# Performance work log

Measured on AMD Instinct MI355X. Metric: run time of the kernel, lower is better.

The kernel has to match this reference:

```python
import jax, jax.numpy as jnp
import numpy as np

NPOINT = 512
NSAMPLE = 32
RADIUS = 0.2


def furthest_point_sampling(pts, npoint):
    # pts: (B, N, 3) -> (B, npoint) int32 indices
    B, N, _ = pts.shape

    def step(carry, _):
        dist, far = carry  # (B,N), (B,)
        centroid = jnp.take_along_axis(pts, far[:, None, None], axis=1)  # (B,1,3)
        d2 = jnp.sum((pts - centroid) ** 2, axis=-1)  # (B,N)
        dist = jnp.minimum(dist, d2)
        nfar = jnp.argmax(dist, axis=-1).astype(jnp.int32)
        return (dist, nfar), far

    init = (jnp.full((B, N), 1e10, pts.dtype), jnp.zeros((B,), jnp.int32))
    _, idxs = jax.lax.scan(step, init, None, length=npoint)
    return idxs.T  # (B, npoint)


def ball_query(new_xyz, xyz, nsample, radius):
    # new_xyz: (B,S,3), xyz: (B,N,3) -> (B,S,nsample) int32
    N = xyz.shape[1]
    d2 = jnp.sum((new_xyz[:, :, None, :] - xyz[:, None, :, :]) ** 2, axis=-1)  # (B,S,N)
    ar = jnp.arange(N, dtype=jnp.int32)
    key = jnp.where(d2 < radius * radius, ar, N)  # valid idx, else sentinel N
    idx = jnp.sort(key, axis=-1)[..., :nsample]  # first nsample in-radius indices
    first = idx[..., :1]
    idx = jnp.where(idx == N, first, idx)  # pad with first valid (CUDA ball_query behavior)
    return jnp.minimum(idx, N - 1)


def group_points(feat, idx):
    # feat: (B,C,N), idx: (B,S,K) -> (B,C,S,K)
    return jax.vmap(lambda f, i: f[:, i])(feat, idx)


def pointnet_sa(xyz, features, W1, b1, W2, b2, W3, b3):
    xyz_t = jnp.transpose(xyz, (0, 2, 1))  # (B,N,3)
    fps_idx = furthest_point_sampling(xyz_t, NPOINT)  # (B,S)
    new_xyz = group_points(xyz, fps_idx[:, :, None])[..., 0]  # (B,3,S)
    idx = ball_query(jnp.transpose(new_xyz, (0, 2, 1)), xyz_t, NSAMPLE, RADIUS)  # (B,S,K)
    grouped_xyz = group_points(xyz, idx) - new_xyz[:, :, :, None]  # (B,3,S,K), centered
    grouped_feat = group_points(features, idx)  # (B,C,S,K)
    h = jnp.concatenate([grouped_xyz, grouped_feat], axis=1)  # (B,C+3,S,K)
    for W, b in ((W1, b1), (W2, b2), (W3, b3)):
        h = jax.nn.relu(jnp.einsum('oc,bcsk->bosk', W, h) + b[None, :, None, None])
    new_features = jnp.max(h, axis=3)  # (B,out,S)
    return new_xyz, new_features


def setup_inputs() -> dict:
    key = jax.random.key(0)
    ks = jax.random.split(key, 8)
    B, N, C = 16, 2048, 64
    return {
        'xyz': jax.random.uniform(ks[0], (B, 3, N), dtype=jnp.float32),
        'features': jax.random.normal(ks[1], (B, C, N), dtype=jnp.float32),
        'W1': jax.random.normal(ks[2], (64, 67), dtype=jnp.float32) * 0.1,
        'b1': jnp.zeros((64,), jnp.float32),
        'W2': jax.random.normal(ks[3], (128, 64), dtype=jnp.float32) * 0.1,
        'b2': jnp.zeros((128,), jnp.float32),
        'W3': jax.random.normal(ks[4], (256, 128), dtype=jnp.float32) * 0.1,
        'b3': jnp.zeros((256,), jnp.float32),
    }


def reference(xyz, features, W1, b1, W2, b2, W3, b3):
    return pointnet_sa(xyz, features, W1, b1, W2, b2, W3, b3)
```

## Files before the change

kernel.cpp:

```cpp
#include <hip/hip_runtime.h>

#define NB 16
#define NN 2048
#define NP 512
#define NS 32
#define NC 64

typedef _Float16 f16x8 __attribute__((ext_vector_type(8)));
typedef _Float16 f16x4 __attribute__((ext_vector_type(4)));
typedef float f32x4 __attribute__((ext_vector_type(4)));
typedef float f32x2 __attribute__((ext_vector_type(2)));

__device__ __forceinline__ float sqdist(float dx, float dy, float dz) {
  return __fadd_rn(__fadd_rn(__fmul_rn(dx, dx), __fmul_rn(dy, dy)), __fmul_rn(dz, dz));
}

__device__ __forceinline__ f32x2 pk_add(f32x2 a, f32x2 b) {
  f32x2 d;
  asm("v_pk_add_f32 %0, %1, %2" : "=v"(d) : "v"(a), "v"(b));
  return d;
}
__device__ __forceinline__ f32x2 pk_mul(f32x2 a, f32x2 b) {
  f32x2 d;
  asm("v_pk_mul_f32 %0, %1, %2" : "=v"(d) : "v"(a), "v"(b));
  return d;
}

template <int CTRL>
__device__ __forceinline__ float dppmaxf(float m) {
  int t = __builtin_amdgcn_update_dpp(0, __float_as_int(m), CTRL, 0xf, 0xf, true);
  return fmaxf(m, __int_as_float(t));
}

__global__ __launch_bounds__(256, 1) void front_kernel(
    const float* __restrict__ xyz, const float* __restrict__ feat,
    const float* __restrict__ W1, const float* __restrict__ W2, const float* __restrict__ W3,
    float* __restrict__ newxyz, _Float16* __restrict__ featF, float* __restrict__ xyzT,
    _Float16* __restrict__ W1f, _Float16* __restrict__ W2f, _Float16* __restrict__ W3f) {
  __shared__ __align__(16) char sm[39040];
  const int bid = blockIdx.x;
  const int t = threadIdx.x;

  if (bid >= 16) {
    if (bid == 528) {
      for (int i = t; i < 256 * 128; i += 256) {
        if (i < 64 * 96) {
          int o = i / 96, k = i - o * 96;
          float v = (k < 64) ? W1[o * 67 + 3 + k] : ((k < 67) ? W1[o * 67 + (k - 64)] : 0.f);
          W1f[i] = (_Float16)v;
        }
        if (i < 128 * 64) W2f[i] = (_Float16)W2[i];
        W3f[i] = (_Float16)W3[i];
      }
      return;
    }
    float(*tile)[65] = (float(*)[65])sm;
    const int pb = bid - 16;
    const int b = pb >> 5;
    const int n0 = (pb & 31) * 64;
    const int g = t >> 6, l = t & 63;
    if (g == 0) {
      int n = n0 + l;
      float4 q;
      q.x = xyz[(size_t)b * 3 * NN + n];
      q.y = xyz[(size_t)b * 3 * NN + NN + n];
      q.z = xyz[(size_t)b * 3 * NN + 2 * NN + n];
      q.w = 0.f;
      ((float4*)xyzT)[(size_t)b * NN + n] = q;
    }
#pragma unroll
    for (int r = 0; r < 16; ++r) {
      int c = g * 16 + r;
      tile[c][l] = feat[((size_t)b * NC + c) * NN + n0 + l];
    }
    __syncthreads();
#pragma unroll
    for (int r = 0; r < 16; ++r) {
      int nl = g * 16 + r;
      featF[((size_t)(b * NN + n0 + nl)) * NC + l] = (_Float16)tile[l][nl];
    }
    return;
  }

  const int b = bid;
  const int w = t >> 6;
  const float* X = xyz + (size_t)b * 3 * NN;
  float4* XL = (float4*)sm;
  float* cst = (float*)(sm + 32768);
  uint2* ck = (uint2*)(sm + 32768 + 6144);

  f32x2 px[4], py[4], pz[4], dist[4];
#pragma unroll
  for (int jj = 0; jj < 4; ++jj) {
    int n0 = t + 256 * jj, n1 = n0 + 1024;
    px[jj] = f32x2{X[n0], X[n1]};
    py[jj] = f32x2{X[NN + n0], X[NN + n1]};
    pz[jj] = f32x2{X[2 * NN + n0], X[2 * NN + n1]};
    dist[jj] = f32x2{1e10f, 1e10f};
    XL[n0] = make_float4(px[jj].x, py[jj].x, pz[jj].x, 0.f);
    XL[n1] = make_float4(px[jj].y, py[jj].y, pz[jj].y, 0.f);
  }
  float cx = X[0], cy = X[NN], cz = X[2 * NN];
  __syncthreads();
  int buf = 0;
  for (int i = 0; i < NP; ++i) {
    if (t == 0) {
      cst[i] = cx;
      cst[NP + i] = cy;
      cst[2 * NP + i] = cz;
    }
    const f32x2 ncx = f32x2{-cx, -cx}, ncy = f32x2{-cy, -cy}, ncz = f32x2{-cz, -cz};
    float hm[4];
#pragma unroll
    for (int jj = 0; jj < 4; ++jj) {
      f32x2 dx = pk_add(px[jj], ncx);
      f32x2 dy = pk_add(py[jj], ncy);
      f32x2 dz = pk_add(pz[jj], ncz);
      f32x2 s = pk_add(pk_add(pk_mul(dx, dx), pk_mul(dy, dy)), pk_mul(dz, dz));
      f32x2 d = dist[jj];
      d.x = fminf(d.x, s.x);
      d.y = fminf(d.y, s.y);
      dist[jj] = d;
      hm[jj] = fmaxf(d.x, d.y);
    }
    float m = fmaxf(fmaxf(hm[0], hm[1]), fmaxf(hm[2], hm[3]));
    m = dppmaxf<0x111>(m);
    m = dppmaxf<0x112>(m);
    m = dppmaxf<0x114>(m);
    m = dppmaxf<0x118>(m);
    m = dppmaxf<0x142>(m);
    m = dppmaxf<0x143>(m);
    const float vmax = __int_as_float(__builtin_amdgcn_readlane(__float_as_int(m), 63));
    unsigned long long mm[8];
#pragma unroll
    for (int jj = 0; jj < 4; ++jj) {
      mm[jj] = __ballot(dist[jj].x == vmax);
      mm[4 + jj] = __ballot(dist[jj].y == vmax);
    }
    unsigned nw = 0;
#pragma unroll
    for (int q = 7; q >= 0; --q)
      if (mm[q]) nw = 256u * (unsigned)q + (unsigned)(w << 6) + (unsigned)__builtin_ctzll(mm[q]);
    if ((t & 63) == 0) ck[buf * 4 + w] = make_uint2(__float_as_uint(vmax), nw);
    __syncthreads();
    uint4 c01 = *(const uint4*)&ck[buf * 4 + 0];
    uint4 c23 = *(const uint4*)&ck[buf * 4 + 2];
    unsigned v = c01.x, n = c01.y;
    if (c01.z > v || (c01.z == v && c01.w < n)) { v = c01.z; n = c01.w; }
    if (c23.x > v || (c23.x == v && c23.y < n)) { v = c23.x; n = c23.y; }
    if (c23.z > v || (c23.z == v && c23.w < n)) { v = c23.z; n = c23.w; }
    float4 c = XL[n];
    cx = c.x;
    cy = c.y;
    cz = c.z;
    buf ^= 1;
  }
  __syncthreads();
  for (int i = t; i < NP; i += 256) {
    newxyz[b * 3 * NP + i] = cst[i];
    newxyz[b * 3 * NP + NP + i] = cst[NP + i];
    newxyz[b * 3 * NP + 2 * NP + i] = cst[2 * NP + i];
  }
}

__global__ __launch_bounds__(256) void ball_kernel(const float* __restrict__ xyz,
                                                   const float* __restrict__ newxyz,
                                                   int* __restrict__ idx) {
  const int b = blockIdx.x;
  const int s = blockIdx.y * 4 + (threadIdx.x >> 6);
  const int lane = threadIdx.x & 63;
  const float* X = xyz + (size_t)b * 3 * NN;
  const float cx = newxyz[b * 3 * NP + s];
  const float cy = newxyz[b * 3 * NP + NP + s];
  const float cz = newxyz[b * 3 * NP + 2 * NP + s];
  int* row = idx + ((size_t)(b * NP + s)) * NS;
  const float r2 = (float)(0.2 * 0.2);
  int total = 0, first = 0;
  bool havefirst = false;
  for (int c0 = 0; c0 < NN; c0 += 64) {
    int n = c0 + lane;
    float d2 = sqdist(X[n] - cx, X[NN + n] - cy, X[2 * NN + n] - cz);
    bool hit = d2 < r2;
    unsigned long long mask = __ballot(hit);
    if (!havefirst && mask) {
      first = c0 + __builtin_ctzll(mask);
      havefirst = true;
    }
    if (hit) {
      int pos = total + (int)__popcll(mask & ((1ull << lane) - 1ull));
      if (pos < NS) row[pos] = n;
    }
    total += (int)__popcll(mask);
    if (total >= NS) break;
  }
  if (total < NS && lane >= total && lane < NS) row[lane] = first;
}

#define HSTR 104
#define A1STR 72
#define A2STR 136
#define A1OFF 17408

__global__ __launch_bounds__(256) void mlp_kernel(
    const float* __restrict__ xyzT, const _Float16* __restrict__ featF,
    const int* __restrict__ idx, const float* __restrict__ newxyz,
    const _Float16* __restrict__ W1f, const float* __restrict__ b1,
    const _Float16* __restrict__ W2f, const float* __restrict__ b2,
    const _Float16* __restrict__ W3f, const float* __restrict__ b3, float* __restrict__ out) {
  __shared__ _Float16 smem[17408 + 9216];
  _Float16* hT = smem;
  _Float16* a1T = smem + A1OFF;
  const int b = blockIdx.x;
  const int s0 = blockIdx.y * 4;
  const int t = threadIdx.x;
  const int lane = t & 63, w = t >> 6;

  {
    const int col = t & 127, hf = t >> 7;
    const int s = s0 + (col >> 5), k = col & 31;
    const int n = idx[((size_t)(b * NP + s)) * NS + k];
    const _Float16* F = featF + (size_t)(b * NN + n) * NC;
#pragma unroll
    for (int j = 0; j < 4; ++j) {
      int p = hf * 4 + j;
      *(f16x8*)(&hT[col * HSTR + p * 8]) = *(const f16x8*)(F + p * 8);
    }
    if (hf == 0) {
      float4 pnt = ((const float4*)xyzT)[(size_t)b * NN + n];
      float cx = newxyz[b * 3 * NP + s];
      float cy = newxyz[b * 3 * NP + NP + s];
      float cz = newxyz[b * 3 * NP + 2 * NP + s];
      f16x8 v = {};
      v[0] = (_Float16)(pnt.x - cx);
      v[1] = (_Float16)(pnt.y - cy);
      v[2] = (_Float16)(pnt.z - cz);
      *(f16x8*)(&hT[col * HSTR + 64]) = v;
    } else {
      f16x8 z = {};
      *(f16x8*)(&hT[col * HSTR + 72]) = z;
      *(f16x8*)(&hT[col * HSTR + 80]) = z;
      *(f16x8*)(&hT[col * HSTR + 88]) = z;
    }
  }
  __syncthreads();

  const int cl = lane & 15;
  const int kg = lane >> 4;

  {
    f32x4 acc[8];
    {
      f32x4 bb = *(const f32x4*)(b1 + w * 16 + kg * 4);
#pragma unroll
      for (int ct = 0; ct < 8; ++ct) acc[ct] = bb;
    }
#pragma unroll
    for (int ks = 0; ks < 3; ++ks) {
      f16x8 A = *(const f16x8*)(W1f + (w * 16 + cl) * 96 + ks * 32 + kg * 8);
#pragma unroll
      for (int ct = 0; ct < 8; ++ct) {
        f16x8 B = *(const f16x8*)(&hT[(ct * 16 + cl) * HSTR + ks * 32 + kg * 8]);
        acc[ct] = __builtin_amdgcn_mfma_f32_16x16x32_f16(A, B, acc[ct], 0, 0, 0);
      }
    }
#pragma unroll
    for (int ct = 0; ct < 8; ++ct) {
      f16x4 v;
#pragma unroll
      for (int i2 = 0; i2 < 4; ++i2) v[i2] = (_Float16)fmaxf(acc[ct][i2], 0.f);
      *(f16x4*)(&a1T[(ct * 16 + cl) * A1STR + w * 16 + kg * 4]) = v;
    }
  }
  __syncthreads();

  {
    f32x4 acc[2][8];
#pragma unroll
    for (int r = 0; r < 2; ++r) {
      f32x4 bb = *(const f32x4*)(b2 + w * 32 + r * 16 + kg * 4);
#pragma unroll
      for (int ct = 0; ct < 8; ++ct) acc[r][ct] = bb;
    }
#pragma unroll
    for (int ks = 0; ks < 2; ++ks) {
      f16x8 A0 = *(const f16x8*)(W2f + (w * 32 + cl) * 64 + ks * 32 + kg * 8);
      f16x8 A1 = *(const f16x8*)(W2f + (w * 32 + 16 + cl) * 64 + ks * 32 + kg * 8);
#pragma unroll
      for (int ct = 0; ct < 8; ++ct) {
        f16x8 B = *(const f16x8*)(&a1T[(ct * 16 + cl) * A1STR + ks * 32 + kg * 8]);
        acc[0][ct] = __builtin_amdgcn_mfma_f32_16x16x32_f16(A0, B, acc[0][ct], 0, 0, 0);
        acc[1][ct] = __builtin_amdgcn_mfma_f32_16x16x32_f16(A1, B, acc[1][ct], 0, 0, 0);
      }
    }
#pragma unroll
    for (int r = 0; r < 2; ++r)
#pragma unroll
      for (int ct = 0; ct < 8; ++ct) {
        f16x4 v;
#pragma unroll
        for (int i2 = 0; i2 < 4; ++i2) v[i2] = (_Float16)fmaxf(acc[r][ct][i2], 0.f);
        *(f16x4*)(&hT[(ct * 16 + cl) * A2STR + w * 32 + r * 16 + kg * 4]) = v;
      }
  }
  __syncthreads();

  float* out2 = out + NB * 3 * NP;
#pragma unroll
  for (int rh = 0; rh < 2; ++rh) {
    f32x4 acc[2][8];
#pragma unroll
    for (int r = 0; r < 2; ++r) {
      f32x4 bb = *(const f32x4*)(b3 + w * 64 + rh * 32 + r * 16 + kg * 4);
#pragma unroll
      for (int ct = 0; ct < 8; ++ct) acc[r][ct] = bb;
    }
#pragma unroll
    for (int ks = 0; ks < 4; ++ks) {
      f16x8 A0 = *(const f16x8*)(W3f + (w * 64 + rh * 32 + cl) * 128 + ks * 32 + kg * 8);
      f16x8 A1 = *(const f16x8*)(W3f + (w * 64 + rh * 32 + 16 + cl) * 128 + ks * 32 + kg * 8);
#pragma unroll
      for (int ct = 0; ct < 8; ++ct) {
        f16x8 B = *(const f16x8*)(&hT[(ct * 16 + cl) * A2STR + ks * 32 + kg * 8]);
        acc[0][ct] = __builtin_amdgcn_mfma_f32_16x16x32_f16(A0, B, acc[0][ct], 0, 0, 0);
        acc[1][ct] = __builtin_amdgcn_mfma_f32_16x16x32_f16(A1, B, acc[1][ct], 0, 0, 0);
      }
    }
#pragma unroll
    for (int r = 0; r < 2; ++r)
#pragma unroll
      for (int sl = 0; sl < 4; ++sl) {
        float vv[4];
#pragma unroll
        for (int i2 = 0; i2 < 4; ++i2) {
          float m0 = fmaxf(acc[r][sl * 2][i2], 0.f);
          float m1 = fmaxf(acc[r][sl * 2 + 1][i2], 0.f);
          float mv = fmaxf(m0, m1);
          mv = fmaxf(mv, __shfl_xor(mv, 1, 64));
          mv = fmaxf(mv, __shfl_xor(mv, 2, 64));
          mv = fmaxf(mv, __shfl_xor(mv, 4, 64));
          mv = fmaxf(mv, __shfl_xor(mv, 8, 64));
          vv[i2] = mv;
        }
        if (cl == 0) {
          int ob = w * 64 + rh * 32 + r * 16 + kg * 4;
#pragma unroll
          for (int i2 = 0; i2 < 4; ++i2)
            out2[((size_t)(b * 256 + ob + i2)) * NP + s0 + sl] = vv[i2];
        }
      }
  }
}

extern "C" void kernel_launch(void* const* d_in, const int* in_sizes, int n_in, void* d_out,
                              int out_size, void* d_ws, size_t ws_size, hipStream_t stream) {
  const float* xyz = (const float*)d_in[0];
  const float* feat = (const float*)d_in[1];
  const float* W1 = (const float*)d_in[2];
  const float* b1 = (const float*)d_in[3];
  const float* W2 = (const float*)d_in[4];
  const float* b2 = (const float*)d_in[5];
  const float* W3 = (const float*)d_in[6];
  const float* b3 = (const float*)d_in[7];
  float* out = (float*)d_out;
  char* ws = (char*)d_ws;
  float* xyzT = (float*)ws;
  _Float16* featF = (_Float16*)(ws + 524288);
  int* idx = (int*)(ws + 4718592);
  _Float16* W1f = (_Float16*)(ws + 5767168);
  _Float16* W2f = (_Float16*)(ws + 5779456);
  _Float16* W3f = (_Float16*)(ws + 5795840);

  hipLaunchKernelGGL(front_kernel, dim3(529), dim3(256), 0, stream, xyz, feat, W1, W2, W3, out,
                     featF, xyzT, W1f, W2f, W3f);
  hipLaunchKernelGGL(ball_kernel, dim3(NB, 128), dim3(256), 0, stream, xyz, out, idx);
  hipLaunchKernelGGL(mlp_kernel, dim3(NB, 128), dim3(256), 0, stream, xyzT, featF, idx, out, W1f,
                     b1, W2f, b2, W3f, b3, out);
}
```

Measured before the change: 378.0 us.

## Fuse ball query into MLP kernel and write FPS centroids directly

Removes the separate ball_kernel launch and performs the ball query inside mlp_kernel, with each wave finding neighbours for one centroid and storing the indices in shared memory rather than a global idx buffer. The FPS loop now writes each centroid straight to global memory instead of staging it in shared memory and copying it out at the end. This drops one launch and a global round-trip of the index array. In exchange, the MLP kernel gains a serial, data-dependent search phase plus an extra barrier before its gather, and the FPS thread issues scattered global stores inside its hot loop.

```diff
diff --git a/kernel.cpp b/kernel.cpp
--- a/kernel.cpp
+++ b/kernel.cpp
@@ -37,7 +37,7 @@
     const float* __restrict__ W1, const float* __restrict__ W2, const float* __restrict__ W3,
     float* __restrict__ newxyz, _Float16* __restrict__ featF, float* __restrict__ xyzT,
     _Float16* __restrict__ W1f, _Float16* __restrict__ W2f, _Float16* __restrict__ W3f) {
-  __shared__ __align__(16) char sm[39040];
+  __shared__ __align__(16) char sm[32896];
   const int bid = blockIdx.x;
   const int t = threadIdx.x;
 
@@ -86,8 +86,7 @@
   const int w = t >> 6;
   const float* X = xyz + (size_t)b * 3 * NN;
   float4* XL = (float4*)sm;
-  float* cst = (float*)(sm + 32768);
-  uint2* ck = (uint2*)(sm + 32768 + 6144);
+  uint2* ck = (uint2*)(sm + 32768);
 
   f32x2 px[4], py[4], pz[4], dist[4];
 #pragma unroll
@@ -105,9 +104,9 @@
   int buf = 0;
   for (int i = 0; i < NP; ++i) {
     if (t == 0) {
-      cst[i] = cx;
-      cst[NP + i] = cy;
-      cst[2 * NP + i] = cz;
+      newxyz[b * 3 * NP + i] = cx;
+      newxyz[b * 3 * NP + NP + i] = cy;
+      newxyz[b * 3 * NP + 2 * NP + i] = cz;
     }
     const f32x2 ncx = f32x2{-cx, -cx}, ncy = f32x2{-cy, -cy}, ncz = f32x2{-cz, -cz};
     float hm[4];
@@ -155,45 +154,6 @@
     cz = c.z;
     buf ^= 1;
   }
-  __syncthreads();
-  for (int i = t; i < NP; i += 256) {
-    newxyz[b * 3 * NP + i] = cst[i];
-    newxyz[b * 3 * NP + NP + i] = cst[NP + i];
-    newxyz[b * 3 * NP + 2 * NP + i] = cst[2 * NP + i];
-  }
-}
-
-__global__ __launch_bounds__(256) void ball_kernel(const float* __restrict__ xyz,
-                                                   const float* __restrict__ newxyz,
-                                                   int* __restrict__ idx) {
-  const int b = blockIdx.x;
-  const int s = blockIdx.y * 4 + (threadIdx.x >> 6);
-  const int lane = threadIdx.x & 63;
-  const float* X = xyz + (size_t)b * 3 * NN;
-  const float cx = newxyz[b * 3 * NP + s];
-  const float cy = newxyz[b * 3 * NP + NP + s];
-  const float cz = newxyz[b * 3 * NP + 2 * NP + s];
-  int* row = idx + ((size_t)(b * NP + s)) * NS;
-  const float r2 = (float)(0.2 * 0.2);
-  int total = 0, first = 0;
-  bool havefirst = false;
-  for (int c0 = 0; c0 < NN; c0 += 64) {
-    int n = c0 + lane;
-    float d2 = sqdist(X[n] - cx, X[NN + n] - cy, X[2 * NN + n] - cz);
-    bool hit = d2 < r2;
-    unsigned long long mask = __ballot(hit);
-    if (!havefirst && mask) {
-      first = c0 + __builtin_ctzll(mask);
-      havefirst = true;
-    }
-    if (hit) {
-      int pos = total + (int)__popcll(mask & ((1ull << lane) - 1ull));
-      if (pos < NS) row[pos] = n;
-    }
-    total += (int)__popcll(mask);
-    if (total >= NS) break;
-  }
-  if (total < NS && lane >= total && lane < NS) row[lane] = first;
 }
 
 #define HSTR 104
@@ -202,12 +162,14 @@
 #define A1OFF 17408
 
 __global__ __launch_bounds__(256) void mlp_kernel(
-    const float* __restrict__ xyzT, const _Float16* __restrict__ featF,
-    const int* __restrict__ idx, const float* __restrict__ newxyz,
+    const float* __restrict__ xyz, const float* __restrict__ xyzT,
+    const _Float16* __restrict__ featF, const float* __restrict__ newxyz,
     const _Float16* __restrict__ W1f, const float* __restrict__ b1,
     const _Float16* __restrict__ W2f, const float* __restrict__ b2,
     const _Float16* __restrict__ W3f, const float* __restrict__ b3, float* __restrict__ out) {
   __shared__ _Float16 smem[17408 + 9216];
+  __shared__ int idx_l[4][32];
+  __shared__ float cxyz[4][4];
   _Float16* hT = smem;
   _Float16* a1T = smem + A1OFF;
   const int b = blockIdx.x;
@@ -216,9 +178,42 @@
   const int lane = t & 63, w = t >> 6;
 
   {
+    const float* X = xyz + (size_t)b * 3 * NN;
+    const int sW = s0 + w;
+    const float cxw = newxyz[b * 3 * NP + sW];
+    const float cyw = newxyz[b * 3 * NP + NP + sW];
+    const float czw = newxyz[b * 3 * NP + 2 * NP + sW];
+    if (lane == 0) {
+      cxyz[w][0] = cxw;
+      cxyz[w][1] = cyw;
+      cxyz[w][2] = czw;
+    }
+    const float r2 = (float)(0.2 * 0.2);
+    int total = 0, first = 0;
+    bool havefirst = false;
+    for (int c0 = 0; c0 < NN; c0 += 64) {
+      int n = c0 + lane;
+      float d2 = sqdist(X[n] - cxw, X[NN + n] - cyw, X[2 * NN + n] - czw);
+      bool hit = d2 < r2;
+      unsigned long long mask = __ballot(hit);
+      if (!havefirst && mask) {
+        first = c0 + __builtin_ctzll(mask);
+        havefirst = true;
+      }
+      if (hit) {
+        int pos = total + (int)__popcll(mask & ((1ull << lane) - 1ull));
+        if (pos < NS) idx_l[w][pos] = n;
+      }
+      total += (int)__popcll(mask);
+      if (total >= NS) break;
+    }
+    if (total < NS && lane >= total && lane < NS) idx_l[w][lane] = first;
+  }
+  __syncthreads();
+
+  {
     const int col = t & 127, hf = t >> 7;
-    const int s = s0 + (col >> 5), k = col & 31;
-    const int n = idx[((size_t)(b * NP + s)) * NS + k];
+    const int n = idx_l[col >> 5][col & 31];
     const _Float16* F = featF + (size_t)(b * NN + n) * NC;
 #pragma unroll
     for (int j = 0; j < 4; ++j) {
@@ -227,13 +222,10 @@
     }
     if (hf == 0) {
       float4 pnt = ((const float4*)xyzT)[(size_t)b * NN + n];
-      float cx = newxyz[b * 3 * NP + s];
-      float cy = newxyz[b * 3 * NP + NP + s];
-      float cz = newxyz[b * 3 * NP + 2 * NP + s];
       f16x8 v = {};
-      v[0] = (_Float16)(pnt.x - cx);
-      v[1] = (_Float16)(pnt.y - cy);
-      v[2] = (_Float16)(pnt.z - cz);
+      v[0] = (_Float16)(pnt.x - cxyz[col >> 5][0]);
+      v[1] = (_Float16)(pnt.y - cxyz[col >> 5][1]);
+      v[2] = (_Float16)(pnt.z - cxyz[col >> 5][2]);
       *(f16x8*)(&hT[col * HSTR + 64]) = v;
     } else {
       f16x8 z = {};
@@ -365,14 +357,12 @@
   char* ws = (char*)d_ws;
   float* xyzT = (float*)ws;
   _Float16* featF = (_Float16*)(ws + 524288);
-  int* idx = (int*)(ws + 4718592);
-  _Float16* W1f = (_Float16*)(ws + 5767168);
-  _Float16* W2f = (_Float16*)(ws + 5779456);
-  _Float16* W3f = (_Float16*)(ws + 5795840);
+  _Float16* W1f = (_Float16*)(ws + 4718592);
+  _Float16* W2f = (_Float16*)(ws + 4730880);
+  _Float16* W3f = (_Float16*)(ws + 4747264);
 
   hipLaunchKernelGGL(front_kernel, dim3(529), dim3(256), 0, stream, xyz, feat, W1, W2, W3, out,
                      featF, xyzT, W1f, W2f, W3f);
-  hipLaunchKernelGGL(ball_kernel, dim3(NB, 128), dim3(256), 0, stream, xyz, out, idx);
-  hipLaunchKernelGGL(mlp_kernel, dim3(NB, 128), dim3(256), 0, stream, xyzT, featF, idx, out, W1f,
+  hipLaunchKernelGGL(mlp_kernel, dim3(NB, 128), dim3(256), 0, stream, xyz, xyzT, featF, out, W1f,
                      b1, W2f, b2, W3f, b3, out);
 }
```

Result: slower. 388.6 us (+2.8%).
